# Kernel tuning notes

Measured on AMD Instinct MI355X. Metric: run time of the kernel, lower is better.

Reference implementation:

```python
import jax, jax.numpy as jnp
import numpy as np

DIM = 512
HEADS = 8
DIM_HEAD = 64
SLICE = 32
INNER = HEADS * DIM_HEAD  # 512


def setup_inputs() -> dict:
    key = jax.random.key(0)
    ks = jax.random.split(key, 8)
    B, N = 8, 8192
    s = 0.02
    return {
        "x": jax.random.normal(ks[0], (B, N, DIM), dtype=jnp.float32),
        "W_in": jax.random.normal(ks[1], (DIM, INNER), dtype=jnp.float32) * s,
        "b_in": jnp.zeros((INNER,), dtype=jnp.float32),
        "Wq": jax.random.normal(ks[2], (DIM_HEAD, SLICE), dtype=jnp.float32) * s,
        "Wk": jax.random.normal(ks[3], (DIM_HEAD, SLICE), dtype=jnp.float32) * s,
        "Wv": jax.random.normal(ks[4], (DIM_HEAD, DIM_HEAD), dtype=jnp.float32) * s,
        "W_out": jax.random.normal(ks[5], (INNER, DIM), dtype=jnp.float32) * s,
        "b_out": jnp.zeros((DIM,), dtype=jnp.float32),
    }


def reference(x, W_in, b_in, Wq, Wk, Wv, W_out, b_out):
    B, N, C = x.shape
    # input projection -> [B, H, N, Dh]
    x_mid = (x @ W_in + b_in).reshape(B, N, HEADS, DIM_HEAD).transpose(0, 2, 1, 3)
    q = x_mid @ Wq            # [B,H,N,S]
    k = x_mid @ Wk            # [B,H,N,S]
    v = x_mid @ Wv            # [B,H,N,Dh]
    q = jax.nn.softmax(q, axis=-1)   # over slice dim
    k = jax.nn.softmax(k, axis=-2)   # over sequence dim
    kv = jnp.einsum('bhns,bhnc->bhsc', k, v)   # [B,H,S,Dh]
    qkv = jnp.einsum('bhns,bhsc->bhnc', q, kv)  # [B,H,N,Dh]
    qkv = qkv.transpose(0, 2, 1, 3).reshape(B, N, INNER)  # b n (h d)
    return qkv @ W_out + b_out
```

## Files before the change

### kernel.cpp

```cpp
#include <hip/hip_runtime.h>
#include <cstdint>
#include <cstddef>

typedef __bf16 bf16_t;
typedef __bf16 bf16x8 __attribute__((ext_vector_type(8)));
typedef __bf16 bf16x4 __attribute__((ext_vector_type(4)));
typedef float  f32x4  __attribute__((ext_vector_type(4)));

#define HEADS    8
#define DIM_HEAD 64
#define SLICE    32
#define DIMC     512
#define NCOL     1024
#define BATCH    8
#define NSEQ     8192
#define NTOK     65536

__device__ __forceinline__ void gl2lds16(const bf16_t* g, bf16_t* l) {
  __builtin_amdgcn_global_load_lds(
      (const __attribute__((address_space(1))) uint32_t*)g,
      (__attribute__((address_space(3))) uint32_t*)l, 16, 0, 0);
}

__global__ __launch_bounds__(256) void xcast_kernel(const float* __restrict__ x,
                                                    bf16_t* __restrict__ xb) {
  const size_t i = ((size_t)blockIdx.x * 256 + threadIdx.x) * 8;
  const float4 a = *reinterpret_cast<const float4*>(x + i);
  const float4 b = *reinterpret_cast<const float4*>(x + i + 4);
  bf16x8 w;
  w[0] = (bf16_t)a.x; w[1] = (bf16_t)a.y; w[2] = (bf16_t)a.z; w[3] = (bf16_t)a.w;
  w[4] = (bf16_t)b.x; w[5] = (bf16_t)b.y; w[6] = (bf16_t)b.z; w[7] = (bf16_t)b.w;
  *reinterpret_cast<bf16x8*>(xb + i) = w;
}

__global__ __launch_bounds__(256) void wprep_kernel(
    const float* __restrict__ W_in, const float* __restrict__ b_in,
    const float* __restrict__ Wq,   const float* __restrict__ Wk,
    const float* __restrict__ Wv,
    bf16_t* __restrict__ WcT, float* __restrict__ bias_c) {
  __shared__ float sW[8192];
  for (int t = threadIdx.x; t < 2048; t += 256) { sW[t] = Wq[t]; sW[2048 + t] = Wk[t]; }
  for (int t = threadIdx.x; t < 4096; t += 256) sW[4096 + t] = Wv[t];
  __syncthreads();

  const int T  = blockIdx.x * 256 + threadIdx.x;
  const int NT = gridDim.x * 256;
  for (int idx = T; idx < NCOL * DIMC; idx += NT) {
    const int col = idx >> 9, cin = idx & 511;
    int base, ldw, h, j;
    if (col < 256)      { h = col >> 5;       j = col & 31;       base = 0;    ldw = 32; }
    else if (col < 512) { h = (col-256) >> 5; j = (col-256) & 31; base = 2048; ldw = 32; }
    else                { h = (col-512) >> 6; j = (col-512) & 63; base = 4096; ldw = 64; }
    const float4* vp = reinterpret_cast<const float4*>(W_in + (size_t)cin * DIMC + h * DIM_HEAD);
    float acc = 0.f;
    #pragma unroll
    for (int d4 = 0; d4 < 16; ++d4) {
      const float4 v = vp[d4];
      acc += v.x * sW[base + (4*d4+0)*ldw + j];
      acc += v.y * sW[base + (4*d4+1)*ldw + j];
      acc += v.z * sW[base + (4*d4+2)*ldw + j];
      acc += v.w * sW[base + (4*d4+3)*ldw + j];
    }
    WcT[(size_t)col * DIMC + cin] = (bf16_t)acc;
  }
  if (T < NCOL) {
    const int col = T;
    int base, ldw, h, j;
    if (col < 256)      { h = col >> 5;       j = col & 31;       base = 0;    ldw = 32; }
    else if (col < 512) { h = (col-256) >> 5; j = (col-256) & 31; base = 2048; ldw = 32; }
    else                { h = (col-512) >> 6; j = (col-512) & 63; base = 4096; ldw = 64; }
    const float* vec = b_in + h * DIM_HEAD;
    float acc = 0.f;
    #pragma unroll 8
    for (int d = 0; d < DIM_HEAD; ++d) acc += vec[d] * sW[base + d * ldw + j];
    bias_c[col] = acc;
  }
}

template<int EPI>
__global__ __launch_bounds__(256) void gemm_kernel(
    const bf16_t* __restrict__ A, const bf16_t* __restrict__ Bt,
    void* __restrict__ Cv, const float* __restrict__ bias,
    int K, int lda, int ldc,
    size_t strideA, size_t strideB, size_t strideC)
{
  __shared__ bf16_t As[128 * 64];
  __shared__ bf16_t Bs[128 * 64];
  const int tid = threadIdx.x;
  const int p = blockIdx.y * gridDim.x + blockIdx.x;
  int mblk, nblk;
  if (EPI == 1) { mblk = (p & 7) + ((p >> 6) << 3); nblk = (p >> 3) & 7; }
  else          { mblk = (p & 7) + ((p >> 5) << 3); nblk = (p >> 3) & 3; }
  const int m0 = mblk * 128;
  const int n0 = nblk * 128;
  const int bz = blockIdx.z;
  const int wave = tid >> 6, lane = tid & 63;
  const int cg   = lane & 15, qd = lane >> 4;
  const int wm   = (wave & 1) * 64, wn = (wave >> 1) * 64;
  const int srow   = lane >> 3;
  const int gchunk = (lane & 7) ^ srow;
  const int chb    = cg & 7;

  const bf16_t* Ab = A  + strideA * bz;
  const bf16_t* Bb = Bt + strideB * bz;

  f32x4 acc[4][4];
  #pragma unroll
  for (int i = 0; i < 4; ++i)
    #pragma unroll
    for (int j = 0; j < 4; ++j) acc[i][j] = (f32x4){0.f, 0.f, 0.f, 0.f};

  for (int k0 = 0; k0 < K; k0 += 64) {
    __syncthreads();
    #pragma unroll
    for (int i = 0; i < 4; ++i) {
      const int c = wave * 4 + i;
      const int row = c * 8 + srow;
      gl2lds16(Ab + (size_t)(m0 + row) * lda + k0 + gchunk * 8, As + c * 512 + lane * 8);
    }
    #pragma unroll
    for (int i = 0; i < 4; ++i) {
      const int c = wave * 4 + i;
      const int row = c * 8 + srow;
      gl2lds16(Bb + (size_t)(n0 + row) * K + k0 + gchunk * 8, Bs + c * 512 + lane * 8);
    }
    __syncthreads();
    #pragma unroll
    for (int ks = 0; ks < 64; ks += 32) {
      const int k4 = ks >> 3;
      bf16x8 af[4], bfr[4];
      #pragma unroll
      for (int i = 0; i < 4; ++i) {
        const int ch = (qd + k4) ^ chb;
        af[i] = *reinterpret_cast<const bf16x8*>(As + (wm + 16*i + cg) * 64 + ch * 8);
      }
      #pragma unroll
      for (int j = 0; j < 4; ++j) {
        const int ch = (qd + k4) ^ chb;
        bfr[j] = *reinterpret_cast<const bf16x8*>(Bs + (wn + 16*j + cg) * 64 + ch * 8);
      }
      #pragma unroll
      for (int i = 0; i < 4; ++i)
        #pragma unroll
        for (int j = 0; j < 4; ++j)
          acc[i][j] = __builtin_amdgcn_mfma_f32_16x16x32_bf16(af[i], bfr[j], acc[i][j], 0, 0, 0);
    }
  }

  if (EPI == 1 && n0 < 256) {
    #pragma unroll
    for (int jp = 0; jp < 2; ++jp) {
      const int j0 = 2 * jp, j1 = 2 * jp + 1;
      const float b0 = bias[n0 + wn + 16 * j0 + cg];
      const float b1 = bias[n0 + wn + 16 * j1 + cg];
      #pragma unroll
      for (int i = 0; i < 4; ++i) {
        #pragma unroll
        for (int rr = 0; rr < 4; ++rr) {
          float v0 = acc[i][j0][rr] + b0;
          float v1 = acc[i][j1][rr] + b1;
          float mx = fmaxf(v0, v1);
          #pragma unroll
          for (int d = 1; d < 16; d <<= 1) mx = fmaxf(mx, __shfl_xor(mx, d, 64));
          const float e0 = __expf(v0 - mx), e1 = __expf(v1 - mx);
          float s = e0 + e1;
          #pragma unroll
          for (int d = 1; d < 16; d <<= 1) s += __shfl_xor(s, d, 64);
          const float rs = 1.f / s;
          const int row = m0 + wm + 16 * i + qd * 4 + rr;
          bf16_t* crow = (bf16_t*)Cv + (size_t)row * ldc;
          crow[n0 + wn + 16 * j0 + cg] = (bf16_t)(e0 * rs);
          crow[n0 + wn + 16 * j1 + cg] = (bf16_t)(e1 * rs);
        }
      }
    }
  } else {
    #pragma unroll
    for (int j = 0; j < 4; ++j) {
      const int col = n0 + wn + 16 * j + cg;
      const float bv = bias[col];
      #pragma unroll
      for (int i = 0; i < 4; ++i) {
        #pragma unroll
        for (int rr = 0; rr < 4; ++rr) {
          const int row = m0 + wm + 16 * i + qd * 4 + rr;
          float v = acc[i][j][rr] + bv;
          if (EPI == 1) {
            if (col < 512) v = __expf(v);
            ((bf16_t*)Cv + strideC * bz)[(size_t)row * ldc + col] = (bf16_t)v;
          } else {
            ((float*)Cv + strideC * bz)[(size_t)row * ldc + col] = v;
          }
        }
      }
    }
  }
}

__global__ __launch_bounds__(256) void kv_accum_kernel(const bf16_t* __restrict__ qkv1,
                                                       float* __restrict__ kv_num,
                                                       float* __restrict__ kv_den) {
  const int chunk = blockIdx.x;
  const int h = blockIdx.y, b = blockIdx.z;
  const int tid = threadIdx.x;
  const int wave = tid >> 6, lane = tid & 63;
  const int cgrp = lane & 15, sgrp = lane >> 4;
  const int c0 = cgrp * 4, s0 = sgrp * 8;

  float acc[8][4];
  float dacc[8];
  #pragma unroll
  for (int i = 0; i < 8; ++i) {
    dacc[i] = 0.f;
    #pragma unroll
    for (int j = 0; j < 4; ++j) acc[i][j] = 0.f;
  }

  const int nbase = chunk * 512 + wave * 128;
  const bf16_t* base = qkv1 + ((size_t)(b * NSEQ + nbase)) * NCOL;
  const int ek_off = 256 + h * SLICE + s0;
  const int v_off  = 512 + h * DIM_HEAD + c0;

  #pragma unroll 4
  for (int n = 0; n < 128; ++n) {
    const bf16_t* rowp = base + (size_t)n * NCOL;
    bf16x8 ek = *reinterpret_cast<const bf16x8*>(rowp + ek_off);
    bf16x4 vv = *reinterpret_cast<const bf16x4*>(rowp + v_off);
    float ekf[8], vf[4];
    #pragma unroll
    for (int i = 0; i < 8; ++i) ekf[i] = (float)ek[i];
    #pragma unroll
    for (int j = 0; j < 4; ++j) vf[j] = (float)vv[j];
    #pragma unroll
    for (int i = 0; i < 8; ++i) {
      dacc[i] += ekf[i];
      #pragma unroll
      for (int j = 0; j < 4; ++j) acc[i][j] += ekf[i] * vf[j];
    }
  }

  __shared__ float red[4][SLICE][DIM_HEAD];
  __shared__ float redd[4][SLICE];
  #pragma unroll
  for (int i = 0; i < 8; ++i)
    #pragma unroll
    for (int j = 0; j < 4; ++j) red[wave][s0 + i][c0 + j] = acc[i][j];
  if (cgrp == 0) {
    #pragma unroll
    for (int i = 0; i < 8; ++i) redd[wave][s0 + i] = dacc[i];
  }
  __syncthreads();
  float* dstn = kv_num + (size_t)(b * HEADS + h) * (SLICE * DIM_HEAD);
  for (int t = tid; t < SLICE * DIM_HEAD; t += 256) {
    const int s = t >> 6, c = t & 63;
    atomicAdd(&dstn[t], red[0][s][c] + red[1][s][c] + red[2][s][c] + red[3][s][c]);
  }
  if (tid < SLICE)
    atomicAdd(&kv_den[(b * HEADS + h) * SLICE + tid],
              redd[0][tid] + redd[1][tid] + redd[2][tid] + redd[3][tid]);
}

__global__ __launch_bounds__(512) void mprep_kernel(const float* __restrict__ kv_num,
                                                    const float* __restrict__ kv_den,
                                                    const float* __restrict__ W_out,
                                                    bf16_t* __restrict__ Mt) {
  const int bh = blockIdx.x, b = bh >> 3, h = bh & 7;
  const int tid = threadIdx.x;
  __shared__ float kvn[SLICE][DIM_HEAD];
  __shared__ float wbuf[8][DIMC];
  const float* src = kv_num + (size_t)bh * (SLICE * DIM_HEAD);
  for (int t = tid; t < SLICE * DIM_HEAD; t += 512)
    kvn[t >> 6][t & 63] = src[t] / kv_den[bh * SLICE + (t >> 6)];
  float accs[SLICE];
  #pragma unroll
  for (int s = 0; s < SLICE; ++s) accs[s] = 0.f;
  for (int cb = 0; cb < DIM_HEAD; cb += 8) {
    __syncthreads();
    for (int t = tid; t < 8 * DIMC; t += 512)
      wbuf[t >> 9][t & 511] = W_out[(size_t)(h * DIM_HEAD + cb + (t >> 9)) * DIMC + (t & 511)];
    __syncthreads();
    #pragma unroll
    for (int cc = 0; cc < 8; ++cc) {
      const float wv = wbuf[cc][tid];
      #pragma unroll
      for (int s = 0; s < SLICE; ++s) accs[s] += kvn[s][cb + cc] * wv;
    }
  }
  bf16_t* dst = Mt + (size_t)b * (DIMC * 256) + (size_t)tid * 256 + h * SLICE;
  #pragma unroll
  for (int s = 0; s < SLICE; ++s) dst[s] = (bf16_t)accs[s];
}

extern "C" void kernel_launch(void* const* d_in, const int* in_sizes, int n_in,
                              void* d_out, int out_size, void* d_ws, size_t ws_size,
                              hipStream_t stream) {
  const float* x     = (const float*)d_in[0];
  const float* W_in  = (const float*)d_in[1];
  const float* b_in  = (const float*)d_in[2];
  const float* Wq    = (const float*)d_in[3];
  const float* Wk    = (const float*)d_in[4];
  const float* Wv    = (const float*)d_in[5];
  const float* W_out = (const float*)d_in[6];
  const float* b_out = (const float*)d_in[7];

  uint8_t* ws = (uint8_t*)d_ws;
  bf16_t* qkv1   = (bf16_t*)(ws);
  bf16_t* WcT    = (bf16_t*)(ws + 134217728ull);
  float*  bias_c = (float*) (ws + 135266304ull);
  float*  kv_num = (float*) (ws + 135270400ull);
  float*  kv_den = (float*) (ws + 135794688ull);
  bf16_t* Mt     = (bf16_t*)(ws + 135802880ull);
  bf16_t* xb = (bf16_t*)d_out;

  hipMemsetAsync(kv_num, 0, 532480, stream);

  xcast_kernel<<<dim3(NTOK * DIMC / 8 / 256), dim3(256), 0, stream>>>(x, xb);
  wprep_kernel<<<dim3(256), dim3(256), 0, stream>>>(W_in, b_in, Wq, Wk, Wv, WcT, bias_c);

  gemm_kernel<1><<<dim3(8, 512, 1), dim3(256), 0, stream>>>(
      xb, WcT, (void*)qkv1, bias_c,
      512 , 512 , NCOL , (size_t)0, (size_t)0, (size_t)0);

  kv_accum_kernel<<<dim3(16, HEADS, BATCH), dim3(256), 0, stream>>>(qkv1, kv_num, kv_den);
  mprep_kernel<<<dim3(BATCH * HEADS), dim3(512), 0, stream>>>(kv_num, kv_den, W_out, Mt);

  gemm_kernel<0><<<dim3(4, 64, BATCH), dim3(256), 0, stream>>>(
      qkv1, Mt, d_out, b_out,
      256 , NCOL , DIMC ,
      (size_t)NSEQ * NCOL, (size_t)DIMC * 256, (size_t)NSEQ * DIMC);
}
```

Before: 521.7 us.

## Fuse K^T·V accumulation into projection GEMM epilogue with head-interleaved columns

Reorders the combined projection weight columns so each 128-column GEMM tile holds one head's q, k and v. The projection GEMM epilogue now computes exp(k) and v into LDS and runs a small MFMA to produce per-tile partial K^T·V and denominators. Only softmaxed q is written to global memory. This removes the large qkv1 intermediate, the separate kv_accum kernel, the atomics and the memset. mprep now reduces 64 partials per (batch, head), and the second GEMM reads a narrower A matrix. The cost is a heavier GEMM epilogue with extra LDS traffic and syncs, plus a larger partial buffer.

```diff
diff --git a/kernel.cpp b/kernel.cpp
--- a/kernel.cpp
+++ b/kernel.cpp
@@ -47,10 +47,11 @@
   const int NT = gridDim.x * 256;
   for (int idx = T; idx < NCOL * DIMC; idx += NT) {
     const int col = idx >> 9, cin = idx & 511;
-    int base, ldw, h, j;
-    if (col < 256)      { h = col >> 5;       j = col & 31;       base = 0;    ldw = 32; }
-    else if (col < 512) { h = (col-256) >> 5; j = (col-256) & 31; base = 2048; ldw = 32; }
-    else                { h = (col-512) >> 6; j = (col-512) & 63; base = 4096; ldw = 64; }
+    const int h = col >> 7, r = col & 127;
+    int base, ldw, j;
+    if (r < 32)      { j = r;      base = 0;    ldw = 32; }
+    else if (r < 64) { j = r - 32; base = 2048; ldw = 32; }
+    else             { j = r - 64; base = 4096; ldw = 64; }
     const float4* vp = reinterpret_cast<const float4*>(W_in + (size_t)cin * DIMC + h * DIM_HEAD);
     float acc = 0.f;
     #pragma unroll
@@ -65,10 +66,11 @@
   }
   if (T < NCOL) {
     const int col = T;
-    int base, ldw, h, j;
-    if (col < 256)      { h = col >> 5;       j = col & 31;       base = 0;    ldw = 32; }
-    else if (col < 512) { h = (col-256) >> 5; j = (col-256) & 31; base = 2048; ldw = 32; }
-    else                { h = (col-512) >> 6; j = (col-512) & 63; base = 4096; ldw = 64; }
+    const int h = col >> 7, r = col & 127;
+    int base, ldw, j;
+    if (r < 32)      { j = r;      base = 0;    ldw = 32; }
+    else if (r < 64) { j = r - 32; base = 2048; ldw = 32; }
+    else             { j = r - 64; base = 4096; ldw = 64; }
     const float* vec = b_in + h * DIM_HEAD;
     float acc = 0.f;
     #pragma unroll 8
@@ -82,7 +84,8 @@
     const bf16_t* __restrict__ A, const bf16_t* __restrict__ Bt,
     void* __restrict__ Cv, const float* __restrict__ bias,
     int K, int lda, int ldc,
-    size_t strideA, size_t strideB, size_t strideC)
+    size_t strideA, size_t strideB, size_t strideC,
+    float* __restrict__ kvp_g, float* __restrict__ denp_g)
 {
   __shared__ bf16_t As[128 * 64];
   __shared__ bf16_t Bs[128 * 64];
@@ -97,8 +100,8 @@
   const int wave = tid >> 6, lane = tid & 63;
   const int cg   = lane & 15, qd = lane >> 4;
   const int wm   = (wave & 1) * 64, wn = (wave >> 1) * 64;
-  const int srow   = lane >> 3;
-  const int gchunk = (lane & 7) ^ srow;
+  const int srw    = lane >> 3;
+  const int gchunk = (lane & 7) ^ srw;
   const int chb    = cg & 7;
 
   const bf16_t* Ab = A  + strideA * bz;
@@ -115,13 +118,13 @@
     #pragma unroll
     for (int i = 0; i < 4; ++i) {
       const int c = wave * 4 + i;
-      const int row = c * 8 + srow;
+      const int row = c * 8 + srw;
       gl2lds16(Ab + (size_t)(m0 + row) * lda + k0 + gchunk * 8, As + c * 512 + lane * 8);
     }
     #pragma unroll
     for (int i = 0; i < 4; ++i) {
       const int c = wave * 4 + i;
-      const int row = c * 8 + srow;
+      const int row = c * 8 + srw;
       gl2lds16(Bb + (size_t)(n0 + row) * K + k0 + gchunk * 8, Bs + c * 512 + lane * 8);
     }
     __syncthreads();
@@ -147,32 +150,99 @@
     }
   }
 
-  if (EPI == 1 && n0 < 256) {
-    #pragma unroll
-    for (int jp = 0; jp < 2; ++jp) {
-      const int j0 = 2 * jp, j1 = 2 * jp + 1;
-      const float b0 = bias[n0 + wn + 16 * j0 + cg];
-      const float b1 = bias[n0 + wn + 16 * j1 + cg];
-      #pragma unroll
-      for (int i = 0; i < 4; ++i) {
-        #pragma unroll
-        for (int rr = 0; rr < 4; ++rr) {
-          float v0 = acc[i][j0][rr] + b0;
-          float v1 = acc[i][j1][rr] + b1;
-          float mx = fmaxf(v0, v1);
+  if (EPI == 1) {
+    const int h   = nblk;
+    const int bat = mblk >> 6;
+    const int mb  = mblk & 63;
+    const int bh  = bat * HEADS + h;
+    __syncthreads();
+    bf16_t* ekT   = As;
+    bf16_t* vT    = Bs;
+    float*  den_s = (float*)(void*)(As + 4096);
+
+    if (wave < 2) {
+      {
+        const float b0 = bias[n0 + cg];
+        const float b1 = bias[n0 + 16 + cg];
+        #pragma unroll
+        for (int i = 0; i < 4; ++i) {
           #pragma unroll
-          for (int d = 1; d < 16; d <<= 1) mx = fmaxf(mx, __shfl_xor(mx, d, 64));
-          const float e0 = __expf(v0 - mx), e1 = __expf(v1 - mx);
-          float s = e0 + e1;
+          for (int rr = 0; rr < 4; ++rr) {
+            float v0 = acc[i][0][rr] + b0;
+            float v1 = acc[i][1][rr] + b1;
+            float mx = fmaxf(v0, v1);
+            #pragma unroll
+            for (int d = 1; d < 16; d <<= 1) mx = fmaxf(mx, __shfl_xor(mx, d, 64));
+            const float e0 = __expf(v0 - mx), e1 = __expf(v1 - mx);
+            float ssum = e0 + e1;
+            #pragma unroll
+            for (int d = 1; d < 16; d <<= 1) ssum += __shfl_xor(ssum, d, 64);
+            const float rs = 1.f / ssum;
+            const int row = m0 + wm + 16 * i + qd * 4 + rr;
+            bf16_t* crow = (bf16_t*)Cv + (size_t)row * ldc + h * SLICE;
+            crow[cg]      = (bf16_t)(e0 * rs);
+            crow[16 + cg] = (bf16_t)(e1 * rs);
+          }
+        }
+      }
+      #pragma unroll
+      for (int j = 2; j < 4; ++j) {
+        const int s = 16 * (j - 2) + cg;
+        const float bb = bias[n0 + 16 * j + cg];
+        float dsum = 0.f;
+        #pragma unroll
+        for (int i = 0; i < 4; ++i) {
           #pragma unroll
-          for (int d = 1; d < 16; d <<= 1) s += __shfl_xor(s, d, 64);
-          const float rs = 1.f / s;
-          const int row = m0 + wm + 16 * i + qd * 4 + rr;
-          bf16_t* crow = (bf16_t*)Cv + (size_t)row * ldc;
-          crow[n0 + wn + 16 * j0 + cg] = (bf16_t)(e0 * rs);
-          crow[n0 + wn + 16 * j1 + cg] = (bf16_t)(e1 * rs);
+          for (int rr = 0; rr < 4; ++rr) {
+            const float e = __expf(acc[i][j][rr] + bb);
+            dsum += e;
+            const int n = wm + 16 * i + qd * 4 + rr;
+            *(bf16_t*)((char*)ekT + (((s << 8) + 2 * n) ^ ((s & 7) << 4))) = (bf16_t)e;
+          }
         }
-      }
+        dsum += __shfl_xor(dsum, 16, 64);
+        dsum += __shfl_xor(dsum, 32, 64);
+        if (qd == 0) den_s[wave * 32 + s] = dsum;
+      }
+    } else {
+      #pragma unroll
+      for (int j = 0; j < 4; ++j) {
+        const int c = 16 * j + cg;
+        const float bb = bias[n0 + 64 + c];
+        #pragma unroll
+        for (int i = 0; i < 4; ++i) {
+          #pragma unroll
+          for (int rr = 0; rr < 4; ++rr) {
+            const float vv = acc[i][j][rr] + bb;
+            const int n = wm + 16 * i + qd * 4 + rr;
+            *(bf16_t*)((char*)vT + (((c << 8) + 2 * n) ^ ((c & 7) << 4))) = (bf16_t)vv;
+          }
+        }
+      }
+    }
+    __syncthreads();
+    if (tid < SLICE)
+      denp_g[((size_t)bh * 64 + mb) * SLICE + tid] = den_s[tid] + den_s[32 + tid];
+
+    const int st = wave & 1;
+    const int sA = st * 16 + cg;
+    float* kvp = kvp_g + ((size_t)bh * 64 + mb) * (SLICE * DIM_HEAD);
+    #pragma unroll
+    for (int ci = 0; ci < 2; ++ci) {
+      const int ct = (wave >> 1) * 2 + ci;
+      const int cB = ct * 16 + cg;
+      f32x4 kacc = (f32x4){0.f, 0.f, 0.f, 0.f};
+      #pragma unroll
+      for (int ks = 0; ks < 4; ++ks) {
+        bf16x8 afr = *(const bf16x8*)((const char*)ekT +
+                       (((sA << 8) + ks * 64 + qd * 16) ^ ((sA & 7) << 4)));
+        bf16x8 bfr2 = *(const bf16x8*)((const char*)vT +
+                       (((cB << 8) + ks * 64 + qd * 16) ^ ((cB & 7) << 4)));
+        kacc = __builtin_amdgcn_mfma_f32_16x16x32_bf16(afr, bfr2, kacc, 0, 0, 0);
+      }
+      #pragma unroll
+      for (int r = 0; r < 4; ++r)
+        kvp[(st * 16 + qd * 4 + r) * DIM_HEAD + ct * 16 + cg] = kacc[r];
     }
   } else {
     #pragma unroll
@@ -184,93 +254,40 @@
         #pragma unroll
         for (int rr = 0; rr < 4; ++rr) {
           const int row = m0 + wm + 16 * i + qd * 4 + rr;
-          float v = acc[i][j][rr] + bv;
-          if (EPI == 1) {
-            if (col < 512) v = __expf(v);
-            ((bf16_t*)Cv + strideC * bz)[(size_t)row * ldc + col] = (bf16_t)v;
-          } else {
-            ((float*)Cv + strideC * bz)[(size_t)row * ldc + col] = v;
-          }
+          ((float*)Cv + strideC * bz)[(size_t)row * ldc + col] = acc[i][j][rr] + bv;
         }
       }
     }
   }
 }
 
-__global__ __launch_bounds__(256) void kv_accum_kernel(const bf16_t* __restrict__ qkv1,
-                                                       float* __restrict__ kv_num,
-                                                       float* __restrict__ kv_den) {
-  const int chunk = blockIdx.x;
-  const int h = blockIdx.y, b = blockIdx.z;
-  const int tid = threadIdx.x;
-  const int wave = tid >> 6, lane = tid & 63;
-  const int cgrp = lane & 15, sgrp = lane >> 4;
-  const int c0 = cgrp * 4, s0 = sgrp * 8;
-
-  float acc[8][4];
-  float dacc[8];
-  #pragma unroll
-  for (int i = 0; i < 8; ++i) {
-    dacc[i] = 0.f;
-    #pragma unroll
-    for (int j = 0; j < 4; ++j) acc[i][j] = 0.f;
-  }
-
-  const int nbase = chunk * 512 + wave * 128;
-  const bf16_t* base = qkv1 + ((size_t)(b * NSEQ + nbase)) * NCOL;
-  const int ek_off = 256 + h * SLICE + s0;
-  const int v_off  = 512 + h * DIM_HEAD + c0;
-
-  #pragma unroll 4
-  for (int n = 0; n < 128; ++n) {
-    const bf16_t* rowp = base + (size_t)n * NCOL;
-    bf16x8 ek = *reinterpret_cast<const bf16x8*>(rowp + ek_off);
-    bf16x4 vv = *reinterpret_cast<const bf16x4*>(rowp + v_off);
-    float ekf[8], vf[4];
-    #pragma unroll
-    for (int i = 0; i < 8; ++i) ekf[i] = (float)ek[i];
-    #pragma unroll
-    for (int j = 0; j < 4; ++j) vf[j] = (float)vv[j];
-    #pragma unroll
-    for (int i = 0; i < 8; ++i) {
-      dacc[i] += ekf[i];
-      #pragma unroll
-      for (int j = 0; j < 4; ++j) acc[i][j] += ekf[i] * vf[j];
-    }
-  }
-
-  __shared__ float red[4][SLICE][DIM_HEAD];
-  __shared__ float redd[4][SLICE];
-  #pragma unroll
-  for (int i = 0; i < 8; ++i)
-    #pragma unroll
-    for (int j = 0; j < 4; ++j) red[wave][s0 + i][c0 + j] = acc[i][j];
-  if (cgrp == 0) {
-    #pragma unroll
-    for (int i = 0; i < 8; ++i) redd[wave][s0 + i] = dacc[i];
-  }
-  __syncthreads();
-  float* dstn = kv_num + (size_t)(b * HEADS + h) * (SLICE * DIM_HEAD);
-  for (int t = tid; t < SLICE * DIM_HEAD; t += 256) {
-    const int s = t >> 6, c = t & 63;
-    atomicAdd(&dstn[t], red[0][s][c] + red[1][s][c] + red[2][s][c] + red[3][s][c]);
-  }
-  if (tid < SLICE)
-    atomicAdd(&kv_den[(b * HEADS + h) * SLICE + tid],
-              redd[0][tid] + redd[1][tid] + redd[2][tid] + redd[3][tid]);
-}
-
-__global__ __launch_bounds__(512) void mprep_kernel(const float* __restrict__ kv_num,
-                                                    const float* __restrict__ kv_den,
+__global__ __launch_bounds__(512) void mprep_kernel(const float* __restrict__ kv_part,
+                                                    const float* __restrict__ den_part,
                                                     const float* __restrict__ W_out,
                                                     bf16_t* __restrict__ Mt) {
-  const int bh = blockIdx.x, b = bh >> 3, h = bh & 7;
+  const int bh = blockIdx.x, bat = bh >> 3, h = bh & 7;
   const int tid = threadIdx.x;
   __shared__ float kvn[SLICE][DIM_HEAD];
+  __shared__ float dsh[SLICE];
   __shared__ float wbuf[8][DIMC];
-  const float* src = kv_num + (size_t)bh * (SLICE * DIM_HEAD);
-  for (int t = tid; t < SLICE * DIM_HEAD; t += 512)
-    kvn[t >> 6][t & 63] = src[t] / kv_den[bh * SLICE + (t >> 6)];
+  const float* np = kv_part + (size_t)bh * 64 * (SLICE * DIM_HEAD);
+  if (tid < SLICE) {
+    const float* dp = den_part + (size_t)bh * 64 * SLICE;
+    float d = 0.f;
+    for (int mb = 0; mb < 64; ++mb) d += dp[mb * SLICE + tid];
+    dsh[tid] = d;
+  }
+  float a0 = 0.f, a1 = 0.f, a2 = 0.f, a3 = 0.f;
+  for (int mb = 0; mb < 64; ++mb) {
+    const float* qp = np + (size_t)mb * (SLICE * DIM_HEAD);
+    a0 += qp[tid]; a1 += qp[tid + 512]; a2 += qp[tid + 1024]; a3 += qp[tid + 1536];
+  }
+  __syncthreads();
+  kvn[tid >> 6][tid & 63]            = a0 / dsh[tid >> 6];
+  kvn[(tid + 512) >> 6][tid & 63]    = a1 / dsh[(tid + 512) >> 6];
+  kvn[(tid + 1024) >> 6][tid & 63]   = a2 / dsh[(tid + 1024) >> 6];
+  kvn[(tid + 1536) >> 6][tid & 63]   = a3 / dsh[(tid + 1536) >> 6];
+
   float accs[SLICE];
   #pragma unroll
   for (int s = 0; s < SLICE; ++s) accs[s] = 0.f;
@@ -286,7 +303,7 @@
       for (int s = 0; s < SLICE; ++s) accs[s] += kvn[s][cb + cc] * wv;
     }
   }
-  bf16_t* dst = Mt + (size_t)b * (DIMC * 256) + (size_t)tid * 256 + h * SLICE;
+  bf16_t* dst = Mt + (size_t)bat * (DIMC * 256) + (size_t)tid * 256 + h * SLICE;
   #pragma unroll
   for (int s = 0; s < SLICE; ++s) dst[s] = (bf16_t)accs[s];
 }
@@ -304,28 +321,27 @@
   const float* b_out = (const float*)d_in[7];
 
   uint8_t* ws = (uint8_t*)d_ws;
-  bf16_t* qkv1   = (bf16_t*)(ws);
-  bf16_t* WcT    = (bf16_t*)(ws + 134217728ull);
-  float*  bias_c = (float*) (ws + 135266304ull);
-  float*  kv_num = (float*) (ws + 135270400ull);
-  float*  kv_den = (float*) (ws + 135794688ull);
-  bf16_t* Mt     = (bf16_t*)(ws + 135802880ull);
+  bf16_t* qprime   = (bf16_t*)(ws);
+  bf16_t* WcT      = (bf16_t*)(ws + 33554432ull);
+  float*  bias_c   = (float*) (ws + 34603008ull);
+  float*  kv_part  = (float*) (ws + 34607104ull);
+  float*  den_part = (float*) (ws + 68161536ull);
+  bf16_t* Mt       = (bf16_t*)(ws + 68685824ull);
   bf16_t* xb = (bf16_t*)d_out;
-
-  hipMemsetAsync(kv_num, 0, 532480, stream);
 
   xcast_kernel<<<dim3(NTOK * DIMC / 8 / 256), dim3(256), 0, stream>>>(x, xb);
   wprep_kernel<<<dim3(256), dim3(256), 0, stream>>>(W_in, b_in, Wq, Wk, Wv, WcT, bias_c);
 
   gemm_kernel<1><<<dim3(8, 512, 1), dim3(256), 0, stream>>>(
-      xb, WcT, (void*)qkv1, bias_c,
-      512 , 512 , NCOL , (size_t)0, (size_t)0, (size_t)0);
-
-  kv_accum_kernel<<<dim3(16, HEADS, BATCH), dim3(256), 0, stream>>>(qkv1, kv_num, kv_den);
-  mprep_kernel<<<dim3(BATCH * HEADS), dim3(512), 0, stream>>>(kv_num, kv_den, W_out, Mt);
+      xb, WcT, (void*)qprime, bias_c,
+      512 , 512 , 256 , (size_t)0, (size_t)0, (size_t)0,
+      kv_part, den_part);
+
+  mprep_kernel<<<dim3(BATCH * HEADS), dim3(512), 0, stream>>>(kv_part, den_part, W_out, Mt);
 
   gemm_kernel<0><<<dim3(4, 64, BATCH), dim3(256), 0, stream>>>(
-      qkv1, Mt, d_out, b_out,
-      256 , NCOL , DIMC ,
-      (size_t)NSEQ * NCOL, (size_t)DIMC * 256, (size_t)NSEQ * DIMC);
-}
+      qprime, Mt, d_out, b_out,
+      256 , 256 , DIMC ,
+      (size_t)NSEQ * 256, (size_t)DIMC * 256, (size_t)NSEQ * DIMC,
+      nullptr, nullptr);
+}
```

After: 451.2 us. 13.5% less time.
